# Optimization experiments

Measured on AMD Instinct MI355X. Metric: run time of the kernel, lower is better.

The kernel has to match this reference:

```python
import jax, jax.numpy as jnp
import numpy as np

IDIM, HDIM, ODIM, G = 80, 512, 128, 5
B, T = 512, 512  # B = scan (time) axis of torch GRU (batch_first=False), T = GRU batch axis
P = G * 2 * ODIM + G  # 1285


def setup_inputs() -> dict:
    key = jax.random.key(0)
    ks = jax.random.split(key, 8)
    s = 0.05  # keep recurrent dynamics stable
    return {
        "ys": jax.random.normal(ks[0], (B, T, IDIM), jnp.float32),
        "W_ih": jax.random.normal(ks[1], (3 * HDIM, IDIM), jnp.float32) * s,
        "W_hh": jax.random.normal(ks[2], (3 * HDIM, HDIM), jnp.float32) * s,
        "b_ih": jax.random.normal(ks[3], (3 * HDIM,), jnp.float32) * s,
        "b_hh": jax.random.normal(ks[4], (3 * HDIM,), jnp.float32) * s,
        "W_proj": jax.random.normal(ks[5], (P, HDIM), jnp.float32) * s,
        "b_proj": jax.random.normal(ks[6], (P,), jnp.float32) * s,
        "eps": jax.random.normal(ks[7], (G, B, ODIM), jnp.float32),  # pre-drawn std-normal noise per component
    }


def _gru(ys, W_ih, W_hh, b_ih, b_hh):
    # torch GRU, batch_first=False: scan over axis 0 of ys, batch = axis 1.
    xp = jnp.einsum('btf,gf->btg', ys, W_ih) + b_ih  # (B, T, 3H), precomputed input projections
    h0 = jnp.zeros((ys.shape[1], HDIM), ys.dtype)

    def step(h, x):
        gh = h @ W_hh.T + b_hh
        xr, xz, xn = jnp.split(x, 3, axis=-1)
        hr, hz, hn = jnp.split(gh, 3, axis=-1)
        r = jax.nn.sigmoid(xr + hr)
        z = jax.nn.sigmoid(xz + hz)
        n = jnp.tanh(xn + r * hn)
        h_new = (1.0 - z) * n + z * h
        return h_new, h_new

    _, out = jax.lax.scan(step, h0, xp)  # (B, T, H)
    return out


def reference(ys, W_ih, W_hh, b_ih, b_hh, W_proj, b_proj, eps):
    out = _gru(ys, W_ih, W_hh, b_ih, b_hh)          # (B, T, H)
    last = out[:, -1, :]                             # (B, H), mirrors out[:, -1, :] in torch code
    params = last @ W_proj.T + b_proj                # (B, P)

    samples = jnp.zeros((ys.shape[0], ODIM), params.dtype)
    for i in range(G):  # tiny fixed component loop (G=5)
        mu = params[:, i * ODIM:(i + 1) * ODIM]                       # (B, odim)
        var = params[:, 2 * i * ODIM:(2 * i + 1) * ODIM] + 1e-6       # scale_tril diagonal == std
        s = jax.lax.stop_gradient(mu + var * eps[i])                  # MVN(mu, diag(var)^T diag(var)).sample()
        w = params[:, 2 * G * ODIM + i]                               # params[:, i - G]
        samples = samples + w[:, None] * s
    return samples[:, None, :]  # (B, 1, odim)
```

## Files before the change

kernel.cpp:

```cpp
#include <hip/hip_runtime.h>
#include <hip/hip_bf16.h>

#define IDIM 80
#define HDIM 512
#define ODIM 128
#define G5   5
#define BB   512
#define TT   512
#define PDIM 1285
#define GDIM 1536
#define NB   48
#define RPB  32
#define PCPB 27

__device__ __forceinline__ void ag_storef(float* p, float v) {
  __hip_atomic_store(p, v, __ATOMIC_RELAXED, __HIP_MEMORY_SCOPE_AGENT);
}
__device__ __forceinline__ float ag_loadf(const float* p) {
  return __hip_atomic_load(p, __ATOMIC_RELAXED, __HIP_MEMORY_SCOPE_AGENT);
}
__device__ __forceinline__ void ag_storeu(unsigned long long* p, unsigned long long v) {
  __hip_atomic_store(p, v, __ATOMIC_RELAXED, __HIP_MEMORY_SCOPE_AGENT);
}
__device__ __forceinline__ unsigned long long ag_loadu(const unsigned long long* p) {
  return __hip_atomic_load(p, __ATOMIC_RELAXED, __HIP_MEMORY_SCOPE_AGENT);
}

__device__ __forceinline__ void grid_barrier(unsigned* bar, unsigned target) {
  __syncthreads();
  if (threadIdx.x == 0) {
    __hip_atomic_fetch_add(bar, 1u, __ATOMIC_ACQ_REL, __HIP_MEMORY_SCOPE_AGENT);
    while (__hip_atomic_load(bar, __ATOMIC_ACQUIRE, __HIP_MEMORY_SCOPE_AGENT) < target) {
      __builtin_amdgcn_s_sleep(1);
    }
  }
  __syncthreads();
}

__global__ void __launch_bounds__(512) gru_kernel(
    const float* __restrict__ ys, const float* __restrict__ W_ih,
    const float* __restrict__ W_hh, const float* __restrict__ b_ih,
    const float* __restrict__ b_hh, const float* __restrict__ W_proj,
    const float* __restrict__ b_proj,
    float* __restrict__ xp, unsigned long long* __restrict__ ghT,
    float* __restrict__ params, unsigned* __restrict__ bar)
{
  const int tid  = threadIdx.x;
  const int nb   = blockIdx.x;
  const int lane = tid & 63;
  const int wave = tid >> 6;
  const int r4   = lane >> 4;
  const int c    = lane & 15;
  const int row  = nb * RPB + wave * 4 + r4;

  __shared__ float hs[2][16 * 36];
  __shared__ float wih[32 * 82];
  __shared__ float bihs[32];

  float4 wreg[8];
  {
    const float4* wrow = (const float4*)(W_hh + (size_t)row * HDIM + c * 32);
    #pragma unroll
    for (int i = 0; i < 8; ++i) wreg[i] = wrow[i];
  }
  const float bhh_r = b_hh[row];

  const int pcol = nb * PCPB + (tid >> 4);
  const int pcl  = tid & 15;
  const bool pact = (tid < 16 * PCPB) && (pcol < PDIM);
  float4 wp[8] = {};
  float bp = 0.f;
  if (pact) {
    const float4* wrow = (const float4*)(W_proj + (size_t)pcol * HDIM + pcl * 32);
    #pragma unroll
    for (int i = 0; i < 8; ++i) wp[i] = wrow[i];
    bp = b_proj[pcol];
  }

  for (int w = tid; w < 16 * 36; w += 512) { hs[0][w] = 0.f; hs[1][w] = 0.f; }

  for (int idx = tid; idx < 32 * IDIM; idx += 512) {
    int g = idx / IDIM, f = idx % IDIM;
    wih[g * 82 + f] = W_ih[(size_t)(nb * RPB + g) * IDIM + f];
  }
  if (tid < 32) bihs[tid] = b_ih[nb * RPB + tid];
  __syncthreads();
  {
    const int g = tid & 31, b0 = tid >> 5;
    for (int pass = 0; pass < 32; ++pass) {
      int b = pass * 16 + b0;
      const float* yrow = ys + ((size_t)b * TT + (TT - 1)) * IDIM;
      float acc = bihs[g];
      #pragma unroll
      for (int f = 0; f < IDIM; f += 2) {
        float2 wv = *(const float2*)(&wih[g * 82 + f]);
        float2 yv = *(const float2*)(&yrow[f]);
        acc += wv.x * yv.x + wv.y * yv.y;
      }
      ag_storef(&xp[(size_t)b * GDIM + nb * RPB + g], acc);
    }
  }
  grid_barrier(bar, NB * 1u);

  const int j = tid;
  const int jphys = (j >> 5) * 36 + (j & 31);

  for (int b = 0; b < BB; ++b) {
    const float* xpb = xp + (size_t)b * GDIM;
    float xr = ag_loadf(&xpb[j]);
    float xz = ag_loadf(&xpb[512 + j]);
    float xn = ag_loadf(&xpb[1024 + j]);

    const float* hbase = &hs[b & 1][c * 36];
    float a0 = 0.f, a1 = 0.f, a2 = 0.f, a3 = 0.f;
    #pragma unroll
    for (int i = 0; i < 8; ++i) {
      float4 h4 = ((const float4*)hbase)[i];
      a0 += wreg[i].x * h4.x; a1 += wreg[i].y * h4.y;
      a2 += wreg[i].z * h4.z; a3 += wreg[i].w * h4.w;
    }
    float acc = (a0 + a1) + (a2 + a3);
    acc += __shfl_xor(acc, 1);
    acc += __shfl_xor(acc, 2);
    acc += __shfl_xor(acc, 4);
    acc += __shfl_xor(acc, 8);
    unsigned long long* ghb = ghT + (size_t)(b & 1) * GDIM;
    if (c == 0) {
      union { float f; unsigned u; } cv; cv.f = acc + bhh_r;
      unsigned long long pv = ((unsigned long long)(unsigned)b << 32) | cv.u;
      ag_storeu(&ghb[row], pv);
    }

    if (b >= 1 && pact) {
      const float* pb = &hs[b & 1][pcl * 36];
      float p0 = 0.f, p1 = 0.f, p2 = 0.f, p3 = 0.f;
      #pragma unroll
      for (int i = 0; i < 8; ++i) {
        float4 h4 = ((const float4*)pb)[i];
        p0 += wp[i].x * h4.x; p1 += wp[i].y * h4.y;
        p2 += wp[i].z * h4.z; p3 += wp[i].w * h4.w;
      }
      float pr = (p0 + p1) + (p2 + p3);
      pr += __shfl_xor(pr, 1);
      pr += __shfl_xor(pr, 2);
      pr += __shfl_xor(pr, 4);
      pr += __shfl_xor(pr, 8);
      if (pcl == 0) params[(size_t)(b - 1) * PDIM + pcol] = pr + bp;
    }

    float hr, hz, hn;
    {
      const unsigned long long* p0 = &ghb[j];
      const unsigned long long* p1 = &ghb[512 + j];
      const unsigned long long* p2 = &ghb[1024 + j];
      unsigned long long v0 = 0, v1 = 0, v2 = 0;
      bool d0 = false, d1 = false, d2 = false;
      int guard = 0;
      do {
        if (!d0) { v0 = ag_loadu(p0); d0 = ((unsigned)(v0 >> 32) == (unsigned)b); }
        if (!d1) { v1 = ag_loadu(p1); d1 = ((unsigned)(v1 >> 32) == (unsigned)b); }
        if (!d2) { v2 = ag_loadu(p2); d2 = ((unsigned)(v2 >> 32) == (unsigned)b); }
      } while ((!d0 || !d1 || !d2) && ++guard < (1 << 20));
      union { unsigned u; float f; } c0, c1, c2;
      c0.u = (unsigned)v0; c1.u = (unsigned)v1; c2.u = (unsigned)v2;
      hr = c0.f; hz = c1.f; hn = c2.f;
    }

    float h_old = hs[b & 1][jphys];
    float r = 1.f / (1.f + __expf(-(xr + hr)));
    float z = 1.f / (1.f + __expf(-(xz + hz)));
    float e2 = __expf(2.f * (xn + r * hn));
    float n = 1.f - 2.f / (e2 + 1.f);
    float hnew = (1.f - z) * n + z * h_old;
    hs[(b + 1) & 1][jphys] = hnew;
    __syncthreads();
  }

  if (pact) {
    const float* pb = &hs[0][pcl * 36];
    float p0 = 0.f, p1 = 0.f, p2 = 0.f, p3 = 0.f;
    #pragma unroll
    for (int i = 0; i < 8; ++i) {
      float4 h4 = ((const float4*)pb)[i];
      p0 += wp[i].x * h4.x; p1 += wp[i].y * h4.y;
      p2 += wp[i].z * h4.z; p3 += wp[i].w * h4.w;
    }
    float pr = (p0 + p1) + (p2 + p3);
    pr += __shfl_xor(pr, 1);
    pr += __shfl_xor(pr, 2);
    pr += __shfl_xor(pr, 4);
    pr += __shfl_xor(pr, 8);
    if (pcl == 0) params[(size_t)(BB - 1) * PDIM + pcol] = pr + bp;
  }
}

__global__ void mix_kernel(const float* __restrict__ params,
                           const float* __restrict__ eps,
                           float* __restrict__ out)
{
  int b = blockIdx.x, o = threadIdx.x;
  const float* pr = params + (size_t)b * PDIM;
  float s = 0.f;
  #pragma unroll
  for (int i = 0; i < G5; ++i) {
    float mu  = pr[i * ODIM + o];
    float var = pr[2 * i * ODIM + o] + 1e-6f;
    float w   = pr[2 * G5 * ODIM + i];
    float e   = eps[((size_t)i * BB + b) * ODIM + o];
    s += w * (mu + var * e);
  }
  out[(size_t)b * ODIM + o] = s;
}

extern "C" void kernel_launch(void* const* d_in, const int* in_sizes, int n_in,
                              void* d_out, int out_size, void* d_ws, size_t ws_size,
                              hipStream_t stream) {
  const float* ys     = (const float*)d_in[0];
  const float* W_ih   = (const float*)d_in[1];
  const float* W_hh   = (const float*)d_in[2];
  const float* b_ih   = (const float*)d_in[3];
  const float* b_hh   = (const float*)d_in[4];
  const float* W_proj = (const float*)d_in[5];
  const float* b_proj = (const float*)d_in[6];
  const float* eps    = (const float*)d_in[7];
  float* out = (float*)d_out;

  char* ws = (char*)d_ws;
  unsigned* bar           = (unsigned*)ws;
  unsigned long long* ghT = (unsigned long long*)(ws + 256);
  float* xp     = (float*)(ws + 256 + 2 * GDIM * 8);
  float* params = xp + (size_t)BB * GDIM;

  hipMemsetAsync(bar, 0, 256, stream);
  hipMemsetAsync(ghT, 0xFF, 2 * GDIM * 8, stream);

  gru_kernel<<<NB, 512, 0, stream>>>(ys, W_ih, W_hh, b_ih, b_hh,
                                     W_proj, b_proj, xp, ghT, params, bar);

  mix_kernel<<<BB, ODIM, 0, stream>>>(params, eps, out);
}
```

Baseline: 1.023 ms.

## Repartition GRU across 16 blocks owning whole hidden units, exchange h instead of gates

Reduces the persistent grid from 48 to 16 blocks. Each block now owns 32 hidden units with all three gate rows, so it can finish the gate nonlinearity locally and publish only the new h value. The flagged global exchange shrinks from three gate values per unit to one h value, padded to separate cache lines. Input projections become block-local, which removes the grid barrier. The trade-off is 32 float4 weight registers per thread, more projection columns per block, and W_proj reread from global memory every step instead of held in registers.

```diff
diff --git a/kernel.cpp b/kernel.cpp
--- a/kernel.cpp
+++ b/kernel.cpp
@@ -9,188 +9,181 @@
 #define TT   512
 #define PDIM 1285
 #define GDIM 1536
-#define NB   48
-#define RPB  32
-#define PCPB 27
-
-__device__ __forceinline__ void ag_storef(float* p, float v) {
-  __hip_atomic_store(p, v, __ATOMIC_RELAXED, __HIP_MEMORY_SCOPE_AGENT);
-}
-__device__ __forceinline__ float ag_loadf(const float* p) {
-  return __hip_atomic_load(p, __ATOMIC_RELAXED, __HIP_MEMORY_SCOPE_AGENT);
-}
-__device__ __forceinline__ void ag_storeu(unsigned long long* p, unsigned long long v) {
-  __hip_atomic_store(p, v, __ATOMIC_RELAXED, __HIP_MEMORY_SCOPE_AGENT);
-}
-__device__ __forceinline__ unsigned long long ag_loadu(const unsigned long long* p) {
-  return __hip_atomic_load(p, __ATOMIC_RELAXED, __HIP_MEMORY_SCOPE_AGENT);
-}
-
-__device__ __forceinline__ void grid_barrier(unsigned* bar, unsigned target) {
-  __syncthreads();
-  if (threadIdx.x == 0) {
-    __hip_atomic_fetch_add(bar, 1u, __ATOMIC_ACQ_REL, __HIP_MEMORY_SCOPE_AGENT);
-    while (__hip_atomic_load(bar, __ATOMIC_ACQUIRE, __HIP_MEMORY_SCOPE_AGENT) < target) {
-      __builtin_amdgcn_s_sleep(1);
-    }
-  }
-  __syncthreads();
-}
+#define NB   16
+#define EPB  32
+#define PCPB 81
+
+__device__ __forceinline__ int PHYS(int j) { return (j >> 5) * 36 + (j & 31); }
 
 __global__ void __launch_bounds__(512) gru_kernel(
     const float* __restrict__ ys, const float* __restrict__ W_ih,
     const float* __restrict__ W_hh, const float* __restrict__ b_ih,
     const float* __restrict__ b_hh, const float* __restrict__ W_proj,
     const float* __restrict__ b_proj,
-    float* __restrict__ xp, unsigned long long* __restrict__ ghT,
-    float* __restrict__ params, unsigned* __restrict__ bar)
+    unsigned long long* __restrict__ hOut, float* __restrict__ xp_loc,
+    float* __restrict__ params)
 {
   const int tid  = threadIdx.x;
   const int nb   = blockIdx.x;
   const int lane = tid & 63;
-  const int wave = tid >> 6;
-  const int r4   = lane >> 4;
-  const int c    = lane & 15;
-  const int row  = nb * RPB + wave * 4 + r4;
+  const int wv   = tid >> 6;
+  const int grpE = lane / 12;
+  const int sub  = lane % 12;
+  const int g    = sub >> 2;
+  const int kq   = lane & 3;
+  const int e    = wv * 4 + grpE;
+  const int jglob = nb * EPB + e;
+  const bool lead = (sub == 0) && (grpE < 4);
 
   __shared__ float hs[2][16 * 36];
-  __shared__ float wih[32 * 82];
-  __shared__ float bihs[32];
-
-  float4 wreg[8];
+  __shared__ float wih[96 * 82];
+  __shared__ float bihs[96];
+
+  int row = g * HDIM + nb * EPB + e; if (row > GDIM - 1) row = GDIM - 1;
+  float4 wreg[32];
   {
-    const float4* wrow = (const float4*)(W_hh + (size_t)row * HDIM + c * 32);
+    const float4* wr = (const float4*)(W_hh + (size_t)row * HDIM) + kq * 32;
     #pragma unroll
-    for (int i = 0; i < 8; ++i) wreg[i] = wrow[i];
-  }
-  const float bhh_r = b_hh[row];
-
-  const int pcol = nb * PCPB + (tid >> 4);
-  const int pcl  = tid & 15;
-  const bool pact = (tid < 16 * PCPB) && (pcol < PDIM);
-  float4 wp[8] = {};
-  float bp = 0.f;
-  if (pact) {
-    const float4* wrow = (const float4*)(W_proj + (size_t)pcol * HDIM + pcl * 32);
-    #pragma unroll
-    for (int i = 0; i < 8; ++i) wp[i] = wrow[i];
-    bp = b_proj[pcol];
-  }
+    for (int i = 0; i < 32; ++i) wreg[i] = wr[i];
+  }
+  const float bias_r = b_hh[row];
 
   for (int w = tid; w < 16 * 36; w += 512) { hs[0][w] = 0.f; hs[1][w] = 0.f; }
 
-  for (int idx = tid; idx < 32 * IDIM; idx += 512) {
-    int g = idx / IDIM, f = idx % IDIM;
-    wih[g * 82 + f] = W_ih[(size_t)(nb * RPB + g) * IDIM + f];
-  }
-  if (tid < 32) bihs[tid] = b_ih[nb * RPB + tid];
+  for (int idx = tid; idx < 96 * IDIM; idx += 512) {
+    int g32 = idx / IDIM, f = idx - g32 * IDIM;
+    int rr = (g32 >> 5) * HDIM + nb * EPB + (g32 & 31);
+    wih[g32 * 82 + f] = W_ih[(size_t)rr * IDIM + f];
+  }
+  if (tid < 96) {
+    int rr = (tid >> 5) * HDIM + nb * EPB + (tid & 31);
+    bihs[tid] = b_ih[rr];
+  }
   __syncthreads();
   {
-    const int g = tid & 31, b0 = tid >> 5;
-    for (int pass = 0; pass < 32; ++pass) {
-      int b = pass * 16 + b0;
-      const float* yrow = ys + ((size_t)b * TT + (TT - 1)) * IDIM;
-      float acc = bihs[g];
-      #pragma unroll
-      for (int f = 0; f < IDIM; f += 2) {
-        float2 wv = *(const float2*)(&wih[g * 82 + f]);
-        float2 yv = *(const float2*)(&yrow[f]);
-        acc += wv.x * yv.x + wv.y * yv.y;
-      }
-      ag_storef(&xp[(size_t)b * GDIM + nb * RPB + g], acc);
-    }
-  }
-  grid_barrier(bar, NB * 1u);
-
-  const int j = tid;
-  const int jphys = (j >> 5) * 36 + (j & 31);
+    const int g5 = tid & 31, bs = tid >> 5;
+    float* xpl = xp_loc + (size_t)nb * BB * 96;
+    for (int gp = 0; gp < 3; ++gp) {
+      int g32 = gp * 32 + g5;
+      for (int pass = 0; pass < 32; ++pass) {
+        int b = pass * 16 + bs;
+        const float* yrow = ys + ((size_t)b * TT + TT - 1) * IDIM;
+        float acc = bihs[g32];
+        #pragma unroll
+        for (int f = 0; f < IDIM; f += 2) {
+          float2 w2 = *(const float2*)&wih[g32 * 82 + f];
+          float2 yv = *(const float2*)&yrow[f];
+          acc += w2.x * yv.x + w2.y * yv.y;
+        }
+        xpl[(size_t)b * 96 + g32] = acc;
+      }
+    }
+  }
+  __syncthreads();
+
+  const float* xpl = xp_loc + (size_t)nb * BB * 96;
+  float xr_c = 0.f, xz_c = 0.f, xn_c = 0.f;
+  if (lead) { xr_c = xpl[e]; xz_c = xpl[32 + e]; xn_c = xpl[64 + e]; }
+
+  const int j  = tid;
+  const int jp = PHYS(j);
 
   for (int b = 0; b < BB; ++b) {
-    const float* xpb = xp + (size_t)b * GDIM;
-    float xr = ag_loadf(&xpb[j]);
-    float xz = ag_loadf(&xpb[512 + j]);
-    float xn = ag_loadf(&xpb[1024 + j]);
-
-    const float* hbase = &hs[b & 1][c * 36];
+    const int cur = b & 1, nxt = cur ^ 1;
+
+    float xr_n = 0.f, xz_n = 0.f, xn_n = 0.f;
+    if (lead && b + 1 < BB) {
+      const float* xq = xpl + (size_t)(b + 1) * 96;
+      xr_n = xq[e]; xz_n = xq[32 + e]; xn_n = xq[64 + e];
+    }
+
     float a0 = 0.f, a1 = 0.f, a2 = 0.f, a3 = 0.f;
     #pragma unroll
-    for (int i = 0; i < 8; ++i) {
-      float4 h4 = ((const float4*)hbase)[i];
-      a0 += wreg[i].x * h4.x; a1 += wreg[i].y * h4.y;
-      a2 += wreg[i].z * h4.z; a3 += wreg[i].w * h4.w;
-    }
-    float acc = (a0 + a1) + (a2 + a3);
-    acc += __shfl_xor(acc, 1);
-    acc += __shfl_xor(acc, 2);
-    acc += __shfl_xor(acc, 4);
-    acc += __shfl_xor(acc, 8);
-    unsigned long long* ghb = ghT + (size_t)(b & 1) * GDIM;
-    if (c == 0) {
-      union { float f; unsigned u; } cv; cv.f = acc + bhh_r;
+    for (int grp = 0; grp < 4; ++grp) {
+      const float4* hb = (const float4*)&hs[cur][(kq * 4 + grp) * 36];
+      #pragma unroll
+      for (int i = 0; i < 8; ++i) {
+        float4 h4 = hb[i]; float4 w4 = wreg[grp * 8 + i];
+        a0 += w4.x * h4.x; a1 += w4.y * h4.y;
+        a2 += w4.z * h4.z; a3 += w4.w * h4.w;
+      }
+    }
+    float dot = (a0 + a1) + (a2 + a3);
+    dot += __shfl_xor(dot, 1);
+    dot += __shfl_xor(dot, 2);
+    dot += bias_r;
+
+    const int base = (lane / 12) * 12;
+    float d1 = __shfl(dot, base + 4);
+    float d2 = __shfl(dot, base + 8);
+
+    if (lead) {
+      float h_old = hs[cur][PHYS(jglob)];
+      float r = 1.f / (1.f + __expf(-(xr_c + dot)));
+      float z = 1.f / (1.f + __expf(-(xz_c + d1)));
+      float e2 = __expf(2.f * (xn_c + r * d2));
+      float n = 1.f - 2.f / (e2 + 1.f);
+      float hnew = (1.f - z) * n + z * h_old;
+      union { float f; unsigned u; } cv; cv.f = hnew;
       unsigned long long pv = ((unsigned long long)(unsigned)b << 32) | cv.u;
-      ag_storeu(&ghb[row], pv);
-    }
-
-    if (b >= 1 && pact) {
-      const float* pb = &hs[b & 1][pcl * 36];
+      __hip_atomic_store(&hOut[((size_t)cur * HDIM + jglob) * 8], pv,
+                         __ATOMIC_RELAXED, __HIP_MEMORY_SCOPE_AGENT);
+    }
+
+    if (b >= 1 && tid < 4 * PCPB) {
+      int col = tid >> 2, kq2 = tid & 3, gcol = nb * PCPB + col;
+      if (gcol < PDIM) {
+        const float4* wp = (const float4*)(W_proj + (size_t)gcol * HDIM) + kq2 * 32;
+        float p0 = 0.f, p1 = 0.f, p2 = 0.f, p3 = 0.f;
+        #pragma unroll
+        for (int grp = 0; grp < 4; ++grp) {
+          const float4* hb = (const float4*)&hs[cur][(kq2 * 4 + grp) * 36];
+          #pragma unroll
+          for (int i = 0; i < 8; ++i) {
+            float4 h4 = hb[i]; float4 w4 = wp[grp * 8 + i];
+            p0 += w4.x * h4.x; p1 += w4.y * h4.y;
+            p2 += w4.z * h4.z; p3 += w4.w * h4.w;
+          }
+        }
+        float pr = (p0 + p1) + (p2 + p3);
+        pr += __shfl_xor(pr, 1);
+        pr += __shfl_xor(pr, 2);
+        if (kq2 == 0) params[(size_t)(b - 1) * PDIM + gcol] = pr + b_proj[gcol];
+      }
+    }
+
+    unsigned long long v; int guard = 0;
+    do {
+      v = __hip_atomic_load(&hOut[((size_t)cur * HDIM + j) * 8],
+                            __ATOMIC_RELAXED, __HIP_MEMORY_SCOPE_AGENT);
+    } while ((unsigned)(v >> 32) != (unsigned)b && ++guard < (1 << 20));
+    union { unsigned u; float f; } hv; hv.u = (unsigned)v;
+    hs[nxt][jp] = hv.f;
+
+    xr_c = xr_n; xz_c = xz_n; xn_c = xn_n;
+    __syncthreads();
+  }
+
+  if (tid < 4 * PCPB) {
+    int col = tid >> 2, kq2 = tid & 3, gcol = nb * PCPB + col;
+    if (gcol < PDIM) {
+      const float4* wp = (const float4*)(W_proj + (size_t)gcol * HDIM) + kq2 * 32;
       float p0 = 0.f, p1 = 0.f, p2 = 0.f, p3 = 0.f;
       #pragma unroll
-      for (int i = 0; i < 8; ++i) {
-        float4 h4 = ((const float4*)pb)[i];
-        p0 += wp[i].x * h4.x; p1 += wp[i].y * h4.y;
-        p2 += wp[i].z * h4.z; p3 += wp[i].w * h4.w;
+      for (int grp = 0; grp < 4; ++grp) {
+        const float4* hb = (const float4*)&hs[0][(kq2 * 4 + grp) * 36];
+        #pragma unroll
+        for (int i = 0; i < 8; ++i) {
+          float4 h4 = hb[i]; float4 w4 = wp[grp * 8 + i];
+          p0 += w4.x * h4.x; p1 += w4.y * h4.y;
+          p2 += w4.z * h4.z; p3 += w4.w * h4.w;
+        }
       }
       float pr = (p0 + p1) + (p2 + p3);
       pr += __shfl_xor(pr, 1);
       pr += __shfl_xor(pr, 2);
-      pr += __shfl_xor(pr, 4);
-      pr += __shfl_xor(pr, 8);
-      if (pcl == 0) params[(size_t)(b - 1) * PDIM + pcol] = pr + bp;
-    }
-
-    float hr, hz, hn;
-    {
-      const unsigned long long* p0 = &ghb[j];
-      const unsigned long long* p1 = &ghb[512 + j];
-      const unsigned long long* p2 = &ghb[1024 + j];
-      unsigned long long v0 = 0, v1 = 0, v2 = 0;
-      bool d0 = false, d1 = false, d2 = false;
-      int guard = 0;
-      do {
-        if (!d0) { v0 = ag_loadu(p0); d0 = ((unsigned)(v0 >> 32) == (unsigned)b); }
-        if (!d1) { v1 = ag_loadu(p1); d1 = ((unsigned)(v1 >> 32) == (unsigned)b); }
-        if (!d2) { v2 = ag_loadu(p2); d2 = ((unsigned)(v2 >> 32) == (unsigned)b); }
-      } while ((!d0 || !d1 || !d2) && ++guard < (1 << 20));
-      union { unsigned u; float f; } c0, c1, c2;
-      c0.u = (unsigned)v0; c1.u = (unsigned)v1; c2.u = (unsigned)v2;
-      hr = c0.f; hz = c1.f; hn = c2.f;
-    }
-
-    float h_old = hs[b & 1][jphys];
-    float r = 1.f / (1.f + __expf(-(xr + hr)));
-    float z = 1.f / (1.f + __expf(-(xz + hz)));
-    float e2 = __expf(2.f * (xn + r * hn));
-    float n = 1.f - 2.f / (e2 + 1.f);
-    float hnew = (1.f - z) * n + z * h_old;
-    hs[(b + 1) & 1][jphys] = hnew;
-    __syncthreads();
-  }
-
-  if (pact) {
-    const float* pb = &hs[0][pcl * 36];
-    float p0 = 0.f, p1 = 0.f, p2 = 0.f, p3 = 0.f;
-    #pragma unroll
-    for (int i = 0; i < 8; ++i) {
-      float4 h4 = ((const float4*)pb)[i];
-      p0 += wp[i].x * h4.x; p1 += wp[i].y * h4.y;
-      p2 += wp[i].z * h4.z; p3 += wp[i].w * h4.w;
-    }
-    float pr = (p0 + p1) + (p2 + p3);
-    pr += __shfl_xor(pr, 1);
-    pr += __shfl_xor(pr, 2);
-    pr += __shfl_xor(pr, 4);
-    pr += __shfl_xor(pr, 8);
-    if (pcl == 0) params[(size_t)(BB - 1) * PDIM + pcol] = pr + bp;
+      if (kq2 == 0) params[(size_t)(BB - 1) * PDIM + gcol] = pr + b_proj[gcol];
+    }
   }
 }
 
@@ -226,16 +219,14 @@
   float* out = (float*)d_out;
 
   char* ws = (char*)d_ws;
-  unsigned* bar           = (unsigned*)ws;
-  unsigned long long* ghT = (unsigned long long*)(ws + 256);
-  float* xp     = (float*)(ws + 256 + 2 * GDIM * 8);
-  float* params = xp + (size_t)BB * GDIM;
-
-  hipMemsetAsync(bar, 0, 256, stream);
-  hipMemsetAsync(ghT, 0xFF, 2 * GDIM * 8, stream);
+  unsigned long long* hOut = (unsigned long long*)ws;
+  float* xp_loc = (float*)(ws + 2 * HDIM * 8 * 8);
+  float* params = xp_loc + (size_t)NB * BB * 96;
+
+  hipMemsetAsync(hOut, 0xFF, 2 * HDIM * 8 * 8, stream);
 
   gru_kernel<<<NB, 512, 0, stream>>>(ys, W_ih, W_hh, b_ih, b_hh,
-                                     W_proj, b_proj, xp, ghT, params, bar);
+                                     W_proj, b_proj, hOut, xp_loc, params);
 
   mix_kernel<<<BB, ODIM, 0, stream>>>(params, eps, out);
 }
```

After: 3.473 ms. 3.39x slower.

## Poll recurrent gate exchange with wide vector loads and stage xp chunks in LDS

Applied to the files above, without the earlier changes.

Each block no longer has all 512 threads poll three 64-bit tagged entries apiece for the shared recurrent gate vector. Now 192 threads poll with four dwordx4 loads each, check every tag, write the values into LDS and then hit a block barrier. The input projections are also loaded 8 timesteps at a time into LDS with inline-asm vector loads, which removes three per-step global atomic loads. The goal is fewer global memory transactions on the serial critical path, at the cost of an extra __syncthreads per step and more LDS use.

```diff
diff --git a/kernel.cpp b/kernel.cpp
--- a/kernel.cpp
+++ b/kernel.cpp
@@ -13,17 +13,13 @@
 #define RPB  32
 #define PCPB 27
 
+typedef unsigned u32x4 __attribute__((ext_vector_type(4)));
+
 __device__ __forceinline__ void ag_storef(float* p, float v) {
   __hip_atomic_store(p, v, __ATOMIC_RELAXED, __HIP_MEMORY_SCOPE_AGENT);
 }
-__device__ __forceinline__ float ag_loadf(const float* p) {
-  return __hip_atomic_load(p, __ATOMIC_RELAXED, __HIP_MEMORY_SCOPE_AGENT);
-}
 __device__ __forceinline__ void ag_storeu(unsigned long long* p, unsigned long long v) {
   __hip_atomic_store(p, v, __ATOMIC_RELAXED, __HIP_MEMORY_SCOPE_AGENT);
-}
-__device__ __forceinline__ unsigned long long ag_loadu(const unsigned long long* p) {
-  return __hip_atomic_load(p, __ATOMIC_RELAXED, __HIP_MEMORY_SCOPE_AGENT);
 }
 
 __device__ __forceinline__ void grid_barrier(unsigned* bar, unsigned target) {
@@ -53,8 +49,9 @@
   const int c    = lane & 15;
   const int row  = nb * RPB + wave * 4 + r4;
 
+  __shared__ float xpl[8 * GDIM];
+  __shared__ float gh_lds[GDIM];
   __shared__ float hs[2][16 * 36];
-  __shared__ float wih[32 * 82];
   __shared__ float bihs[32];
 
   float4 wreg[8];
@@ -79,13 +76,14 @@
 
   for (int w = tid; w < 16 * 36; w += 512) { hs[0][w] = 0.f; hs[1][w] = 0.f; }
 
-  for (int idx = tid; idx < 32 * IDIM; idx += 512) {
-    int g = idx / IDIM, f = idx % IDIM;
-    wih[g * 82 + f] = W_ih[(size_t)(nb * RPB + g) * IDIM + f];
-  }
-  if (tid < 32) bihs[tid] = b_ih[nb * RPB + tid];
-  __syncthreads();
   {
+    float* wih = xpl;
+    for (int idx = tid; idx < 32 * IDIM; idx += 512) {
+      int g = idx / IDIM, f = idx % IDIM;
+      wih[g * 82 + f] = W_ih[(size_t)(nb * RPB + g) * IDIM + f];
+    }
+    if (tid < 32) bihs[tid] = b_ih[nb * RPB + tid];
+    __syncthreads();
     const int g = tid & 31, b0 = tid >> 5;
     for (int pass = 0; pass < 32; ++pass) {
       int b = pass * 16 + b0;
@@ -106,12 +104,39 @@
   const int jphys = (j >> 5) * 36 + (j & 31);
 
   for (int b = 0; b < BB; ++b) {
-    const float* xpb = xp + (size_t)b * GDIM;
-    float xr = ag_loadf(&xpb[j]);
-    float xz = ag_loadf(&xpb[512 + j]);
-    float xn = ag_loadf(&xpb[1024 + j]);
-
-    const float* hbase = &hs[b & 1][c * 36];
+    const int cur = b & 1, nxt = cur ^ 1;
+
+    if ((b & 7) == 0) {
+      const float* base = xp + (size_t)b * GDIM;
+      unsigned long long a0 = (unsigned long long)(base + (0 * 512 + tid) * 4);
+      unsigned long long a1 = (unsigned long long)(base + (1 * 512 + tid) * 4);
+      unsigned long long a2 = (unsigned long long)(base + (2 * 512 + tid) * 4);
+      unsigned long long a3 = (unsigned long long)(base + (3 * 512 + tid) * 4);
+      unsigned long long a4 = (unsigned long long)(base + (4 * 512 + tid) * 4);
+      unsigned long long a5 = (unsigned long long)(base + (5 * 512 + tid) * 4);
+      u32x4 q0, q1, q2, q3, q4, q5;
+      asm volatile(
+        "global_load_dwordx4 %0, %6, off sc1\n\t"
+        "global_load_dwordx4 %1, %7, off sc1\n\t"
+        "global_load_dwordx4 %2, %8, off sc1\n\t"
+        "global_load_dwordx4 %3, %9, off sc1\n\t"
+        "global_load_dwordx4 %4, %10, off sc1\n\t"
+        "global_load_dwordx4 %5, %11, off sc1\n\t"
+        "s_waitcnt vmcnt(0)"
+        : "=&v"(q0), "=&v"(q1), "=&v"(q2), "=&v"(q3), "=&v"(q4), "=&v"(q5)
+        : "v"(a0), "v"(a1), "v"(a2), "v"(a3), "v"(a4), "v"(a5)
+        : "memory");
+      union { u32x4 u; float4 f; } cv;
+      float4* dst = (float4*)xpl;
+      cv.u = q0; dst[0 * 512 + tid] = cv.f;
+      cv.u = q1; dst[1 * 512 + tid] = cv.f;
+      cv.u = q2; dst[2 * 512 + tid] = cv.f;
+      cv.u = q3; dst[3 * 512 + tid] = cv.f;
+      cv.u = q4; dst[4 * 512 + tid] = cv.f;
+      cv.u = q5; dst[5 * 512 + tid] = cv.f;
+    }
+
+    const float* hbase = &hs[cur][c * 36];
     float a0 = 0.f, a1 = 0.f, a2 = 0.f, a3 = 0.f;
     #pragma unroll
     for (int i = 0; i < 8; ++i) {
@@ -124,7 +149,7 @@
     acc += __shfl_xor(acc, 2);
     acc += __shfl_xor(acc, 4);
     acc += __shfl_xor(acc, 8);
-    unsigned long long* ghb = ghT + (size_t)(b & 1) * GDIM;
+    unsigned long long* ghb = ghT + (size_t)cur * GDIM;
     if (c == 0) {
       union { float f; unsigned u; } cv; cv.f = acc + bhh_r;
       unsigned long long pv = ((unsigned long long)(unsigned)b << 32) | cv.u;
@@ -132,7 +157,7 @@
     }
 
     if (b >= 1 && pact) {
-      const float* pb = &hs[b & 1][pcl * 36];
+      const float* pb = &hs[cur][pcl * 36];
       float p0 = 0.f, p1 = 0.f, p2 = 0.f, p3 = 0.f;
       #pragma unroll
       for (int i = 0; i < 8; ++i) {
@@ -148,31 +173,50 @@
       if (pcl == 0) params[(size_t)(b - 1) * PDIM + pcol] = pr + bp;
     }
 
-    float hr, hz, hn;
+    if (tid < 192) {
+      unsigned long long la = (unsigned long long)(ghb + (size_t)tid * 8);
+      const unsigned bb = (unsigned)b;
+      int guard = 0;
+      for (;;) {
+        u32x4 A, B, C, D;
+        asm volatile(
+          "global_load_dwordx4 %0, %4, off sc1\n\t"
+          "global_load_dwordx4 %1, %4, off offset:16 sc1\n\t"
+          "global_load_dwordx4 %2, %4, off offset:32 sc1\n\t"
+          "global_load_dwordx4 %3, %4, off offset:48 sc1\n\t"
+          "s_waitcnt vmcnt(0)"
+          : "=&v"(A), "=&v"(B), "=&v"(C), "=&v"(D) : "v"(la) : "memory");
+        bool ok = (A.y == bb) & (A.w == bb) & (B.y == bb) & (B.w == bb)
+                & (C.y == bb) & (C.w == bb) & (D.y == bb) & (D.w == bb);
+        if (ok) {
+          union { unsigned u; float f; } t;
+          float4 v0, v1;
+          t.u = A.x; v0.x = t.f; t.u = A.z; v0.y = t.f;
+          t.u = B.x; v0.z = t.f; t.u = B.z; v0.w = t.f;
+          t.u = C.x; v1.x = t.f; t.u = C.z; v1.y = t.f;
+          t.u = D.x; v1.z = t.f; t.u = D.z; v1.w = t.f;
+          float4* g4 = (float4*)(gh_lds + tid * 8);
+          g4[0] = v0; g4[1] = v1;
+          break;
+        }
+        if (++guard >= (1 << 20)) break;
+        __builtin_amdgcn_s_sleep(1);
+      }
+    }
+    __syncthreads();
+
     {
-      const unsigned long long* p0 = &ghb[j];
-      const unsigned long long* p1 = &ghb[512 + j];
-      const unsigned long long* p2 = &ghb[1024 + j];
-      unsigned long long v0 = 0, v1 = 0, v2 = 0;
-      bool d0 = false, d1 = false, d2 = false;
-      int guard = 0;
-      do {
-        if (!d0) { v0 = ag_loadu(p0); d0 = ((unsigned)(v0 >> 32) == (unsigned)b); }
-        if (!d1) { v1 = ag_loadu(p1); d1 = ((unsigned)(v1 >> 32) == (unsigned)b); }
-        if (!d2) { v2 = ag_loadu(p2); d2 = ((unsigned)(v2 >> 32) == (unsigned)b); }
-      } while ((!d0 || !d1 || !d2) && ++guard < (1 << 20));
-      union { unsigned u; float f; } c0, c1, c2;
-      c0.u = (unsigned)v0; c1.u = (unsigned)v1; c2.u = (unsigned)v2;
-      hr = c0.f; hz = c1.f; hn = c2.f;
-    }
-
-    float h_old = hs[b & 1][jphys];
-    float r = 1.f / (1.f + __expf(-(xr + hr)));
-    float z = 1.f / (1.f + __expf(-(xz + hz)));
-    float e2 = __expf(2.f * (xn + r * hn));
-    float n = 1.f - 2.f / (e2 + 1.f);
-    float hnew = (1.f - z) * n + z * h_old;
-    hs[(b + 1) & 1][jphys] = hnew;
+      const float* xs = xpl + (size_t)(b & 7) * GDIM;
+      float xr = xs[j], xz = xs[512 + j], xn = xs[1024 + j];
+      float hr = gh_lds[j], hz = gh_lds[512 + j], hn = gh_lds[1024 + j];
+      float h_old = hs[cur][jphys];
+      float r = 1.f / (1.f + __expf(-(xr + hr)));
+      float z = 1.f / (1.f + __expf(-(xz + hz)));
+      float e2 = __expf(2.f * (xn + r * hn));
+      float n = 1.f - 2.f / (e2 + 1.f);
+      float hnew = (1.f - z) * n + z * h_old;
+      hs[nxt][jphys] = hnew;
+    }
     __syncthreads();
   }
 
```

New measurement: 1.232 ms. +20.4%, slower.
